# Performance work log

Hardware: AMD Instinct MI355X
Metric: run time of the kernel (lower is better)

The kernel has to match this reference:

```python
import jax, jax.numpy as jnp
import numpy as np

B, S, D, H = 8, 1024, 1024, 16
HD = D // H  # head dim 64
NUM_REL = 7


def setup_inputs() -> dict:
    key = jax.random.key(0)
    ks = jax.random.split(key, 10)
    s = 0.02
    return {
        "hidden_states": jax.random.normal(ks[0], (B, S, D), dtype=jnp.float32),
        "attention_mask": jnp.zeros((B, 1, 1, S), dtype=jnp.float32),
        "relation": jax.random.randint(ks[1], (B, S, S), 0, NUM_REL, dtype=jnp.int32),
        "Wq": jax.random.normal(ks[2], (D, D), dtype=jnp.float32) * s,
        "bq": jnp.zeros((D,), dtype=jnp.float32),
        "Wk": jax.random.normal(ks[3], (D, D), dtype=jnp.float32) * s,
        "bk": jnp.zeros((D,), dtype=jnp.float32),
        "Wv": jax.random.normal(ks[4], (D, D), dtype=jnp.float32) * s,
        "bv": jnp.zeros((D,), dtype=jnp.float32),
        "rel_emb": jax.random.normal(ks[5], (NUM_REL, H), dtype=jnp.float32) * s,
    }


def reference(hidden_states, attention_mask, relation, Wq, bq, Wk, bk, Wv, bv, rel_emb):
    def heads(x):  # [B,S,D] -> [B,H,S,HD]
        return x.reshape(B, S, H, HD).transpose(0, 2, 1, 3)

    q = heads(hidden_states @ Wq.T + bq)
    k = heads(hidden_states @ Wk.T + bk)
    v = heads(hidden_states @ Wv.T + bv)

    scores = jnp.einsum("bhqd,bhkd->bhqk", q, k) / jnp.sqrt(jnp.float32(HD))
    # relation bias: gather [B,S,S,H] then move H to dim 1
    rel_bias = rel_emb[relation].transpose(0, 3, 1, 2)  # [B,H,S,S]
    scores = scores + rel_bias + attention_mask
    probs = jax.nn.softmax(scores, axis=-1)  # dropout is identity in eval
    ctx = jnp.einsum("bhqk,bhkd->bhqd", probs, v)
    return ctx.transpose(0, 2, 1, 3).reshape(B, S, D)
```

## Files before the change

### kernel.cpp

```cpp
#include <hip/hip_runtime.h>

#define NB 8
#define NS 1024
#define ND 1024
#define NH 16
#define NHD 64

typedef __attribute__((ext_vector_type(8))) short bf16x8;
typedef __attribute__((ext_vector_type(4))) float f32x4;
typedef __attribute__((ext_vector_type(4))) unsigned int u32x4;

#define GLOAD_LDS16(g, l) __builtin_amdgcn_global_load_lds(                    \
    (const __attribute__((address_space(1))) void*)(g),                        \
    (__attribute__((address_space(3))) void*)(l), 16, 0, 0)

static __device__ __forceinline__ unsigned short f2bf(float f) {
    unsigned int u = __builtin_bit_cast(unsigned int, f);
    unsigned int r = u + 0x7fffu + ((u >> 16) & 1u);
    return (unsigned short)(r >> 16);
}

static __device__ __forceinline__ unsigned int cvtpk(float lo, float hi) {
    unsigned int r;
    asm("v_cvt_pk_bf16_f32 %0, %1, %2" : "=v"(r) : "v"(lo), "v"(hi));
    return r;
}

__global__ void cvt_f32_bf16(const float* __restrict__ in, unsigned short* __restrict__ out, int n) {
    int i = (blockIdx.x * blockDim.x + threadIdx.x) * 4;
    if (i >= n) return;
    float4 v = *reinterpret_cast<const float4*>(in + i);
    ushort4 o;
    o.x = f2bf(v.x); o.y = f2bf(v.y); o.z = f2bf(v.z); o.w = f2bf(v.w);
    *reinterpret_cast<ushort4*>(out + i) = o;
}

__global__ void cvt_w3(const float* __restrict__ Wq, const float* __restrict__ Wk,
                       const float* __restrict__ Wv, unsigned short* __restrict__ out) {
    const float* src = (blockIdx.y == 0) ? Wq : (blockIdx.y == 1) ? Wk : Wv;
    int i = (blockIdx.x * blockDim.x + threadIdx.x) * 4;
    float4 v = *reinterpret_cast<const float4*>(src + i);
    ushort4 o;
    o.x = f2bf(v.x); o.y = f2bf(v.y); o.z = f2bf(v.z); o.w = f2bf(v.w);
    *reinterpret_cast<ushort4*>(out + (size_t)blockIdx.y * (ND * ND) + i) = o;
}

__global__ __launch_bounds__(256) void qkv_gemm(
    const unsigned short* __restrict__ A,
    const unsigned short* __restrict__ Wq, const unsigned short* __restrict__ Wk,
    const unsigned short* __restrict__ Wv,
    const float* __restrict__ bq, const float* __restrict__ bk, const float* __restrict__ bv,
    unsigned short* __restrict__ Qo, unsigned short* __restrict__ Ko, unsigned short* __restrict__ Vo)
{
    const int z = blockIdx.z;
    const unsigned short* W = (z == 0) ? Wq : (z == 1) ? Wk : Wv;
    const float* bias = (z == 0) ? bq : (z == 1) ? bk : bv;
    const int m0 = blockIdx.x * 128;
    const int n0 = blockIdx.y * 128;

    __shared__ unsigned short As[128][64];
    __shared__ unsigned short Bs[128][64];

    const int tid = threadIdx.x;
    const int lane = tid & 63;
    const int wave = tid >> 6;
    const int wm = wave >> 1, wn = wave & 1;

    f32x4 acc[4][4] = {};

    const int crow = lane >> 3;
    const int gcol = ((lane & 7) ^ crow) * 8;
    const int kofs = (lane >> 4) * 8;

    for (int kb = 0; kb < ND; kb += 64) {
#pragma unroll
        for (int cc = 0; cc < 4; ++cc) {
            int c = wave * 4 + cc;
            GLOAD_LDS16(&A[(size_t)(m0 + c * 8 + crow) * ND + kb + gcol], &As[c * 8][0]);
            GLOAD_LDS16(&W[(size_t)(n0 + c * 8 + crow) * ND + kb + gcol], &Bs[c * 8][0]);
        }
        __syncthreads();
#pragma unroll
        for (int kk = 0; kk < 2; ++kk) {
            const int colx = (kk * 32 + kofs) ^ ((lane & 7) * 8);
            bf16x8 af[4], bfr[4];
#pragma unroll
            for (int i = 0; i < 4; ++i) {
                af[i]  = *reinterpret_cast<const bf16x8*>(&As[wm * 64 + i * 16 + (lane & 15)][colx]);
                bfr[i] = *reinterpret_cast<const bf16x8*>(&Bs[wn * 64 + i * 16 + (lane & 15)][colx]);
            }
#pragma unroll
            for (int mi = 0; mi < 4; ++mi)
#pragma unroll
                for (int ni = 0; ni < 4; ++ni)
                    acc[mi][ni] = __builtin_amdgcn_mfma_f32_16x16x32_bf16(af[mi], bfr[ni], acc[mi][ni], 0, 0, 0);
        }
        __syncthreads();
    }

#pragma unroll
    for (int ni = 0; ni < 4; ++ni) {
        int n = n0 + wn * 64 + ni * 16 + (lane & 15);
        float bv_ = bias[n];
        int h = n >> 6, hd = n & 63;
#pragma unroll
        for (int mi = 0; mi < 4; ++mi) {
            int m = m0 + wm * 64 + mi * 16 + (lane >> 4) * 4;
            int b = m >> 10, s = m & 1023;
            if (z == 2) {
                ushort4 o;
                o.x = f2bf(acc[mi][ni][0] + bv_);
                o.y = f2bf(acc[mi][ni][1] + bv_);
                o.z = f2bf(acc[mi][ni][2] + bv_);
                o.w = f2bf(acc[mi][ni][3] + bv_);
                *reinterpret_cast<ushort4*>(&Vo[(((size_t)b * NH + h) * NHD + hd) * NS + s]) = o;
            } else {
                unsigned short* O = (z == 0) ? Qo : Ko;
#pragma unroll
                for (int r2 = 0; r2 < 4; ++r2)
                    O[(((size_t)b * NH + h) * NS + s + r2) * NHD + hd] = f2bf(acc[mi][ni][r2] + bv_);
            }
        }
    }
}

__global__ __launch_bounds__(512) void flash_attn(
    const unsigned short* __restrict__ Q, const unsigned short* __restrict__ Kb,
    const unsigned short* __restrict__ Vt,
    const int* __restrict__ rel, const float* __restrict__ rel_emb,
    const float* __restrict__ mask, float* __restrict__ out)
{
    const int q0 = blockIdx.x * 128;
    const int h = blockIdx.y;
    const int b = blockIdx.z;
    const int tid = threadIdx.x, lane = tid & 63, wave = tid >> 6;
    const int g = lane >> 4, l15 = lane & 15;

    __shared__ unsigned short Ks[2][64][64];
    __shared__ unsigned short Vs[2][64][64];
    __shared__ float s_mask[NS];
    __shared__ float s_re2[8];
    const float LOG2E = 1.4426950408889634f;
    const float SCL2 = 0.125f * 1.4426950408889634f;
    if (tid < 7) s_re2[tid] = rel_emb[tid * NH + h] * LOG2E - 4.0f;

    const unsigned short* Qh = Q  + (((size_t)b * NH + h) * NS) * NHD;
    const unsigned short* Kh = Kb + (((size_t)b * NH + h) * NS) * NHD;
    const unsigned short* Vh = Vt + (((size_t)b * NH + h) * NHD) * NS;
    const int qg = q0 + wave * 16 + l15;
    const int* __restrict__ relrow = rel + (size_t)b * NS * NS + (size_t)qg * NS;
    const float* __restrict__ maskb = mask + (size_t)b * NS;

    bf16x8 qa[2];
    qa[0] = *reinterpret_cast<const bf16x8*>(&Qh[(size_t)qg * NHD + g * 8]);
    qa[1] = *reinterpret_cast<const bf16x8*>(&Qh[(size_t)qg * NHD + 32 + g * 8]);

    bf16x8 vone;
#pragma unroll
    for (int i = 0; i < 8; ++i) vone[i] = (short)0x3F80;

    f32x4 ctx[4] = {};
    f32x4 l_acc = {};
    float mofs = 0.f;
    bool everscaled = false;

    const int crow = lane >> 3;
    const int gcol = ((lane & 7) ^ crow) * 8;
    const int swz8 = (lane & 7) * 8;

    const int rho = wave * 8 + crow;
    const int kvperm = ((rho >> 5) << 5) + (((rho >> 2) & 3) << 3)
                     + (((rho >> 4) & 1) << 2) + (rho & 3);

#define STAGE(buf, kv)                                                                          \
    {                                                                                           \
        GLOAD_LDS16(&Kh[(size_t)((kv) + kvperm) * NHD + gcol], &Ks[buf][wave * 8][0]);          \
        GLOAD_LDS16(&Vh[(size_t)(wave * 8 + crow) * NS + (kv) + gcol], &Vs[buf][wave * 8][0]);  \
    }

#define LOADRM(S, t0)                                                           \
    {                                                                           \
        rc##S[0] = *reinterpret_cast<const int4*>(&relrow[(t0) * 64 + 8 * g]);      \
        rc##S[1] = *reinterpret_cast<const int4*>(&relrow[(t0) * 64 + 8 * g + 4]);  \
        rc##S[2] = *reinterpret_cast<const int4*>(&relrow[(t0) * 64 + 8 * g + 32]); \
        rc##S[3] = *reinterpret_cast<const int4*>(&relrow[(t0) * 64 + 8 * g + 36]); \
    }

#define TILEBAR()                                              \
    {                                                          \
        asm volatile("s_waitcnt vmcnt(4) lgkmcnt(0)" ::: "memory"); \
        __builtin_amdgcn_sched_barrier(0);                     \
        __builtin_amdgcn_s_barrier();                          \
        __builtin_amdgcn_sched_barrier(0);                     \
    }

    int4 rcA[4], rcB[4];

    __builtin_amdgcn_sched_barrier(0);
    STAGE(0, 0)
    __builtin_amdgcn_sched_barrier(0);
    LOADRM(A, 0)
    s_mask[tid] = maskb[tid] * LOG2E;
    s_mask[tid + 512] = maskb[tid + 512] * LOG2E;
    TILEBAR()

#define BODY(cur, S, SN, tc, tn)                                               \
  {                                                                            \
    if ((tn) < 16) {                                                           \
      STAGE(cur ^ 1, (tn) * 64)                                                \
      __builtin_amdgcn_sched_barrier(0);                                       \
      LOADRM(SN, tn)                                                           \
    }                                                                          \
    f32x4 sc[4] = {};                                                          \
    __builtin_amdgcn_s_setprio(1);                                             \
    _Pragma("unroll")                                                          \
    for (int kk = 0; kk < 2; ++kk) {                                           \
      const int colx = (kk * 32 + g * 8) ^ swz8;                               \
      _Pragma("unroll")                                                        \
      for (int tt = 0; tt < 4; ++tt) {                                         \
        bf16x8 kfrag = *reinterpret_cast<const bf16x8*>(&Ks[cur][tt * 16 + l15][colx]); \
        sc[tt] = __builtin_amdgcn_mfma_f32_16x16x32_bf16(kfrag, qa[kk], sc[tt], 0, 0, 0); \
      }                                                                        \
    }                                                                          \
    __builtin_amdgcn_s_setprio(0);                                             \
    float pmax = -1e30f;                                                       \
    _Pragma("unroll")                                                          \
    for (int tt = 0; tt < 4; ++tt) {                                           \
      float4 mv = *reinterpret_cast<const float4*>(                            \
          &s_mask[(tc) * 64 + ((tt >> 1) << 5) + 8 * g + ((tt & 1) << 2)]);    \
      const int rca[4] = {rc##S[tt].x, rc##S[tt].y, rc##S[tt].z, rc##S[tt].w}; \
      float v0 = fmaf(sc[tt][0], SCL2, s_re2[rca[0]] + mv.x);                  \
      float v1 = fmaf(sc[tt][1], SCL2, s_re2[rca[1]] + mv.y);                  \
      float v2 = fmaf(sc[tt][2], SCL2, s_re2[rca[2]] + mv.z);                  \
      float v3 = fmaf(sc[tt][3], SCL2, s_re2[rca[3]] + mv.w);                  \
      sc[tt][0] = v0; sc[tt][1] = v1; sc[tt][2] = v2; sc[tt][3] = v3;          \
      pmax = fmaxf(pmax, fmaxf(fmaxf(v0, v1), fmaxf(v2, v3)));                 \
    }                                                                          \
    if (!__all(pmax <= mofs + 8.0f)) {                                         \
      float pm = fmaxf(pmax, __shfl_xor(pmax, 16));                            \
      pm = fmaxf(pm, __shfl_xor(pm, 32));                                      \
      float mnew = fmaxf(mofs, pm);                                            \
      float alpha = exp2f(mofs - mnew);                                        \
      mofs = mnew;                                                             \
      everscaled = true;                                                       \
      float ar[4];                                                             \
      _Pragma("unroll")                                                        \
      for (int r = 0; r < 4; ++r) ar[r] = __shfl(alpha, 4 * g + r);            \
      _Pragma("unroll")                                                        \
      for (int r = 0; r < 4; ++r) l_acc[r] *= ar[r];                           \
      _Pragma("unroll")                                                        \
      for (int ht = 0; ht < 4; ++ht)                                           \
        _Pragma("unroll")                                                      \
        for (int r = 0; r < 4; ++r) ctx[ht][r] *= ar[r];                       \
    }                                                                          \
    unsigned int pw[8];                                                        \
    if (!everscaled) {                                                         \
      _Pragma("unroll")                                                        \
      for (int tt = 0; tt < 4; ++tt) {                                         \
        pw[2 * tt]     = cvtpk(exp2f(sc[tt][0]), exp2f(sc[tt][1]));            \
        pw[2 * tt + 1] = cvtpk(exp2f(sc[tt][2]), exp2f(sc[tt][3]));            \
      }                                                                        \
    } else {                                                                   \
      _Pragma("unroll")                                                        \
      for (int tt = 0; tt < 4; ++tt) {                                         \
        pw[2 * tt]     = cvtpk(exp2f(sc[tt][0] - mofs), exp2f(sc[tt][1] - mofs)); \
        pw[2 * tt + 1] = cvtpk(exp2f(sc[tt][2] - mofs), exp2f(sc[tt][3] - mofs)); \
      }                                                                        \
    }                                                                          \
    __builtin_amdgcn_s_setprio(1);                                             \
    _Pragma("unroll")                                                          \
    for (int kk = 0; kk < 2; ++kk) {                                           \
      u32x4 paw = {pw[4 * kk], pw[4 * kk + 1], pw[4 * kk + 2], pw[4 * kk + 3]};\
      bf16x8 pa = __builtin_bit_cast(bf16x8, paw);                             \
      const int colx = (kk * 32 + g * 8) ^ swz8;                               \
      l_acc = __builtin_amdgcn_mfma_f32_16x16x32_bf16(pa, vone, l_acc, 0, 0, 0); \
      _Pragma("unroll")                                                        \
      for (int ht = 0; ht < 4; ++ht) {                                         \
        bf16x8 bfrag = *reinterpret_cast<const bf16x8*>(&Vs[cur][ht * 16 + l15][colx]); \
        ctx[ht] = __builtin_amdgcn_mfma_f32_16x16x32_bf16(pa, bfrag, ctx[ht], 0, 0, 0); \
      }                                                                        \
    }                                                                          \
    __builtin_amdgcn_s_setprio(0);                                             \
    TILEBAR()                                                                  \
  }

    for (int t = 0; t < 16; t += 2) {
        BODY(0, A, B, t, t + 1)
        BODY(1, B, A, t + 1, t + 2)
    }
#undef BODY
#undef LOADRM
#undef STAGE
#undef TILEBAR

    float linv[4];
#pragma unroll
    for (int r = 0; r < 4; ++r) linv[r] = 1.0f / l_acc[r];
#pragma unroll
    for (int ht = 0; ht < 4; ++ht) {
        int hd = ht * 16 + l15;
#pragma unroll
        for (int r = 0; r < 4; ++r) {
            int qo = q0 + wave * 16 + 4 * g + r;
            out[((size_t)b * NS + qo) * ND + h * NHD + hd] = ctx[ht][r] * linv[r];
        }
    }
}

extern "C" void kernel_launch(void* const* d_in, const int* in_sizes, int n_in,
                              void* d_out, int out_size, void* d_ws, size_t ws_size,
                              hipStream_t stream) {
    const float* hs      = (const float*)d_in[0];
    const float* mask    = (const float*)d_in[1];
    const int*   rel     = (const int*)d_in[2];
    const float* Wq      = (const float*)d_in[3];
    const float* bq      = (const float*)d_in[4];
    const float* Wk      = (const float*)d_in[5];
    const float* bk      = (const float*)d_in[6];
    const float* Wv      = (const float*)d_in[7];
    const float* bv      = (const float*)d_in[8];
    const float* rel_emb = (const float*)d_in[9];
    float* out = (float*)d_out;

    char* ws = (char*)d_ws;
    unsigned short* q_bf  = (unsigned short*)(ws);
    unsigned short* k_bf  = (unsigned short*)(ws + ((size_t)16 << 20));
    unsigned short* vt_bf = (unsigned short*)(ws + ((size_t)32 << 20));
    unsigned short* hs_bf = (unsigned short*)(ws + ((size_t)48 << 20));
    unsigned short* w_bf  = (unsigned short*)(ws + ((size_t)64 << 20));

    const int nhs = NB * NS * ND;
    const int nw  = ND * ND;
    cvt_f32_bf16<<<nhs / 4 / 256, 256, 0, stream>>>(hs, hs_bf, nhs);
    cvt_w3<<<dim3(nw / 4 / 256, 3), 256, 0, stream>>>(Wq, Wk, Wv, w_bf);

    qkv_gemm<<<dim3((NB * NS) / 128, ND / 128, 3), 256, 0, stream>>>(
        hs_bf, w_bf, w_bf + (size_t)nw, w_bf + (size_t)2 * nw,
        bq, bk, bv, q_bf, k_bf, vt_bf);

    flash_attn<<<dim3(NS / 128, NH, NB), 512, 0, stream>>>(
        q_bf, k_bf, vt_bf, rel, rel_emb, mask, out);
}
```

Baseline: 179.7 us.

## Pack relation indices to bytes and fold the mask into V and the row sums

Adds a pre-pass that packs the int32 relation tensor into uint8. The attention kernel now reads 4x fewer relation bytes per head, and it re-reads that tensor once for each of the 16 heads. The additive mask is moved out of the score loop: V is pre-scaled by exp(mask) in the QKV GEMM epilogue, and the row-sum MFMA uses a bf16 exp(mask) vector instead of ones. The custom waitcnt/sched_barrier tile barriers are also replaced with plain __syncthreads. This costs an extra kernel launch and a 32MB read. The mask factorization loses precision for large negative masks and does not subtract the mask when tracking the row max.

```diff
diff --git a/kernel.cpp b/kernel.cpp
--- a/kernel.cpp
+++ b/kernel.cpp
@@ -45,11 +45,18 @@
     *reinterpret_cast<ushort4*>(out + (size_t)blockIdx.y * (ND * ND) + i) = o;
 }
 
+__global__ void pack_rel8(const int* __restrict__ rel, unsigned int* __restrict__ out) {
+    int i = blockIdx.x * blockDim.x + threadIdx.x;
+    int4 v = reinterpret_cast<const int4*>(rel)[i];
+    out[i] = (unsigned)v.x | ((unsigned)v.y << 8) | ((unsigned)v.z << 16) | ((unsigned)v.w << 24);
+}
+
 __global__ __launch_bounds__(256) void qkv_gemm(
     const unsigned short* __restrict__ A,
     const unsigned short* __restrict__ Wq, const unsigned short* __restrict__ Wk,
     const unsigned short* __restrict__ Wv,
     const float* __restrict__ bq, const float* __restrict__ bk, const float* __restrict__ bv,
+    const float* __restrict__ mask,
     unsigned short* __restrict__ Qo, unsigned short* __restrict__ Ko, unsigned short* __restrict__ Vo)
 {
     const int z = blockIdx.z;
@@ -57,6 +64,7 @@
     const float* bias = (z == 0) ? bq : (z == 1) ? bk : bv;
     const int m0 = blockIdx.x * 128;
     const int n0 = blockIdx.y * 128;
+    const float LOG2E = 1.4426950408889634f;
 
     __shared__ unsigned short As[128][64];
     __shared__ unsigned short Bs[128][64];
@@ -108,11 +116,12 @@
             int m = m0 + wm * 64 + mi * 16 + (lane >> 4) * 4;
             int b = m >> 10, s = m & 1023;
             if (z == 2) {
+                float4 mv = *reinterpret_cast<const float4*>(&mask[(size_t)b * NS + s]);
                 ushort4 o;
-                o.x = f2bf(acc[mi][ni][0] + bv_);
-                o.y = f2bf(acc[mi][ni][1] + bv_);
-                o.z = f2bf(acc[mi][ni][2] + bv_);
-                o.w = f2bf(acc[mi][ni][3] + bv_);
+                o.x = f2bf((acc[mi][ni][0] + bv_) * exp2f(mv.x * LOG2E));
+                o.y = f2bf((acc[mi][ni][1] + bv_) * exp2f(mv.y * LOG2E));
+                o.z = f2bf((acc[mi][ni][2] + bv_) * exp2f(mv.z * LOG2E));
+                o.w = f2bf((acc[mi][ni][3] + bv_) * exp2f(mv.w * LOG2E));
                 *reinterpret_cast<ushort4*>(&Vo[(((size_t)b * NH + h) * NHD + hd) * NS + s]) = o;
             } else {
                 unsigned short* O = (z == 0) ? Qo : Ko;
@@ -127,7 +136,7 @@
 __global__ __launch_bounds__(512) void flash_attn(
     const unsigned short* __restrict__ Q, const unsigned short* __restrict__ Kb,
     const unsigned short* __restrict__ Vt,
-    const int* __restrict__ rel, const float* __restrict__ rel_emb,
+    const unsigned char* __restrict__ rel8, const float* __restrict__ rel_emb,
     const float* __restrict__ mask, float* __restrict__ out)
 {
     const int q0 = blockIdx.x * 128;
@@ -138,7 +147,7 @@
 
     __shared__ unsigned short Ks[2][64][64];
     __shared__ unsigned short Vs[2][64][64];
-    __shared__ float s_mask[NS];
+    __shared__ unsigned short s_emask[NS];
     __shared__ float s_re2[8];
     const float LOG2E = 1.4426950408889634f;
     const float SCL2 = 0.125f * 1.4426950408889634f;
@@ -148,16 +157,12 @@
     const unsigned short* Kh = Kb + (((size_t)b * NH + h) * NS) * NHD;
     const unsigned short* Vh = Vt + (((size_t)b * NH + h) * NHD) * NS;
     const int qg = q0 + wave * 16 + l15;
-    const int* __restrict__ relrow = rel + (size_t)b * NS * NS + (size_t)qg * NS;
+    const unsigned char* __restrict__ relrow = rel8 + (size_t)b * NS * NS + (size_t)qg * NS;
     const float* __restrict__ maskb = mask + (size_t)b * NS;
 
     bf16x8 qa[2];
     qa[0] = *reinterpret_cast<const bf16x8*>(&Qh[(size_t)qg * NHD + g * 8]);
     qa[1] = *reinterpret_cast<const bf16x8*>(&Qh[(size_t)qg * NHD + 32 + g * 8]);
-
-    bf16x8 vone;
-#pragma unroll
-    for (int i = 0; i < 8; ++i) vone[i] = (short)0x3F80;
 
     f32x4 ctx[4] = {};
     f32x4 l_acc = {};
@@ -178,37 +183,24 @@
         GLOAD_LDS16(&Vh[(size_t)(wave * 8 + crow) * NS + (kv) + gcol], &Vs[buf][wave * 8][0]);  \
     }
 
-#define LOADRM(S, t0)                                                           \
-    {                                                                           \
-        rc##S[0] = *reinterpret_cast<const int4*>(&relrow[(t0) * 64 + 8 * g]);      \
-        rc##S[1] = *reinterpret_cast<const int4*>(&relrow[(t0) * 64 + 8 * g + 4]);  \
-        rc##S[2] = *reinterpret_cast<const int4*>(&relrow[(t0) * 64 + 8 * g + 32]); \
-        rc##S[3] = *reinterpret_cast<const int4*>(&relrow[(t0) * 64 + 8 * g + 36]); \
-    }
-
-#define TILEBAR()                                              \
-    {                                                          \
-        asm volatile("s_waitcnt vmcnt(4) lgkmcnt(0)" ::: "memory"); \
-        __builtin_amdgcn_sched_barrier(0);                     \
-        __builtin_amdgcn_s_barrier();                          \
-        __builtin_amdgcn_sched_barrier(0);                     \
-    }
-
-    int4 rcA[4], rcB[4];
-
-    __builtin_amdgcn_sched_barrier(0);
+#define LOADRM(S, t0)                                                                \
+    {                                                                                \
+        r##S##a = *reinterpret_cast<const uint2*>(&relrow[(t0) * 64 + 8 * g]);       \
+        r##S##b = *reinterpret_cast<const uint2*>(&relrow[(t0) * 64 + 32 + 8 * g]);  \
+    }
+
+    uint2 rAa, rAb, rBa, rBb;
+
     STAGE(0, 0)
-    __builtin_amdgcn_sched_barrier(0);
     LOADRM(A, 0)
-    s_mask[tid] = maskb[tid] * LOG2E;
-    s_mask[tid + 512] = maskb[tid + 512] * LOG2E;
-    TILEBAR()
+    s_emask[tid] = f2bf(exp2f(maskb[tid] * LOG2E));
+    s_emask[tid + 512] = f2bf(exp2f(maskb[tid + 512] * LOG2E));
+    __syncthreads();
 
 #define BODY(cur, S, SN, tc, tn)                                               \
   {                                                                            \
     if ((tn) < 16) {                                                           \
       STAGE(cur ^ 1, (tn) * 64)                                                \
-      __builtin_amdgcn_sched_barrier(0);                                       \
       LOADRM(SN, tn)                                                           \
     }                                                                          \
     f32x4 sc[4] = {};                                                          \
@@ -223,16 +215,14 @@
       }                                                                        \
     }                                                                          \
     __builtin_amdgcn_s_setprio(0);                                             \
+    const unsigned int rw[4] = {r##S##a.x, r##S##a.y, r##S##b.x, r##S##b.y};   \
     float pmax = -1e30f;                                                       \
     _Pragma("unroll")                                                          \
     for (int tt = 0; tt < 4; ++tt) {                                           \
-      float4 mv = *reinterpret_cast<const float4*>(                            \
-          &s_mask[(tc) * 64 + ((tt >> 1) << 5) + 8 * g + ((tt & 1) << 2)]);    \
-      const int rca[4] = {rc##S[tt].x, rc##S[tt].y, rc##S[tt].z, rc##S[tt].w}; \
-      float v0 = fmaf(sc[tt][0], SCL2, s_re2[rca[0]] + mv.x);                  \
-      float v1 = fmaf(sc[tt][1], SCL2, s_re2[rca[1]] + mv.y);                  \
-      float v2 = fmaf(sc[tt][2], SCL2, s_re2[rca[2]] + mv.z);                  \
-      float v3 = fmaf(sc[tt][3], SCL2, s_re2[rca[3]] + mv.w);                  \
+      float v0 = fmaf(sc[tt][0], SCL2, s_re2[rw[tt] & 0xFF]);                  \
+      float v1 = fmaf(sc[tt][1], SCL2, s_re2[(rw[tt] >> 8) & 0xFF]);           \
+      float v2 = fmaf(sc[tt][2], SCL2, s_re2[(rw[tt] >> 16) & 0xFF]);          \
+      float v3 = fmaf(sc[tt][3], SCL2, s_re2[rw[tt] >> 24]);                   \
       sc[tt][0] = v0; sc[tt][1] = v1; sc[tt][2] = v2; sc[tt][3] = v3;          \
       pmax = fmaxf(pmax, fmaxf(fmaxf(v0, v1), fmaxf(v2, v3)));                 \
     }                                                                          \
@@ -273,7 +263,8 @@
       u32x4 paw = {pw[4 * kk], pw[4 * kk + 1], pw[4 * kk + 2], pw[4 * kk + 3]};\
       bf16x8 pa = __builtin_bit_cast(bf16x8, paw);                             \
       const int colx = (kk * 32 + g * 8) ^ swz8;                               \
-      l_acc = __builtin_amdgcn_mfma_f32_16x16x32_bf16(pa, vone, l_acc, 0, 0, 0); \
+      bf16x8 mfr = *reinterpret_cast<const bf16x8*>(&s_emask[(tc) * 64 + kk * 32 + g * 8]); \
+      l_acc = __builtin_amdgcn_mfma_f32_16x16x32_bf16(pa, mfr, l_acc, 0, 0, 0); \
       _Pragma("unroll")                                                        \
       for (int ht = 0; ht < 4; ++ht) {                                         \
         bf16x8 bfrag = *reinterpret_cast<const bf16x8*>(&Vs[cur][ht * 16 + l15][colx]); \
@@ -281,7 +272,7 @@
       }                                                                        \
     }                                                                          \
     __builtin_amdgcn_s_setprio(0);                                             \
-    TILEBAR()                                                                  \
+    __syncthreads();                                                           \
   }
 
     for (int t = 0; t < 16; t += 2) {
@@ -291,7 +282,6 @@
 #undef BODY
 #undef LOADRM
 #undef STAGE
-#undef TILEBAR
 
     float linv[4];
 #pragma unroll
@@ -328,6 +318,7 @@
     unsigned short* vt_bf = (unsigned short*)(ws + ((size_t)32 << 20));
     unsigned short* hs_bf = (unsigned short*)(ws + ((size_t)48 << 20));
     unsigned short* w_bf  = (unsigned short*)(ws + ((size_t)64 << 20));
+    unsigned char*  rel8  = (unsigned char*)(ws + ((size_t)48 << 20));
 
     const int nhs = NB * NS * ND;
     const int nw  = ND * ND;
@@ -336,8 +327,10 @@
 
     qkv_gemm<<<dim3((NB * NS) / 128, ND / 128, 3), 256, 0, stream>>>(
         hs_bf, w_bf, w_bf + (size_t)nw, w_bf + (size_t)2 * nw,
-        bq, bk, bv, q_bf, k_bf, vt_bf);
+        bq, bk, bv, mask, q_bf, k_bf, vt_bf);
+
+    pack_rel8<<<(NB * NS * NS / 4) / 256, 256, 0, stream>>>(rel, (unsigned int*)rel8);
 
     flash_attn<<<dim3(NS / 128, NH, NB), 512, 0, stream>>>(
-        q_bf, k_bf, vt_bf, rel, rel_emb, mask, out);
-}
+        q_bf, k_bf, vt_bf, rel8, rel_emb, mask, out);
+}
```

New measurement: 169.2 us. 5.9% less time.
